# Optimization experiments

Hardware: AMD Instinct MI355X
Metric: run time of the kernel (lower is better)

The kernel has to match this reference:

```python
import jax, jax.numpy as jnp
import numpy as np

VNUM = 50000
D = 256
NE = 1600000


def setup_inputs() -> dict:
    key = jax.random.key(0)
    ks = jax.random.split(key, 10)
    return {
        "vrepr": jax.random.normal(ks[0], (VNUM, D), dtype=jnp.float32) * 0.1,
        "sidx": jax.random.randint(ks[1], (NE,), 0, VNUM, dtype=jnp.int32),
        "tidx": jax.random.randint(ks[2], (NE,), 0, VNUM, dtype=jnp.int32),
        "esgn": jnp.where(jax.random.uniform(ks[3], (NE,)) < 0.5, -1.0, 1.0).astype(jnp.float32),
        "enorm": jax.random.uniform(ks[4], (NE,), dtype=jnp.float32),
        "loc_w": jax.random.normal(ks[5], (D, D), dtype=jnp.float32) / np.sqrt(D),
        "loc_b": jax.random.normal(ks[6], (D,), dtype=jnp.float32) * 0.01,
        "std_w": jax.random.normal(ks[7], (D, D), dtype=jnp.float32) / np.sqrt(D),
        "std_b": jax.random.normal(ks[8], (D,), dtype=jnp.float32) * 0.01,
        "eps": jax.random.normal(ks[9], (VNUM, D), dtype=jnp.float32),
    }


def reference(vrepr, sidx, tidx, esgn, enorm, loc_w, loc_b, std_w, std_b, eps):
    # GraphConv: gather source node features, weight by enorm*esgn, scatter-add to targets
    w = (enorm * esgn)[:, None]              # [E, 1]
    msg = vrepr[sidx] * w                    # [E, D]
    ptr = jax.ops.segment_sum(msg, tidx, num_segments=vrepr.shape[0])  # [V, D]
    # Linear heads (torch Linear: y = x @ W.T + b)
    loc = ptr @ loc_w.T + loc_b
    std = jax.nn.softplus(ptr @ std_w.T + std_b) + 1e-7
    # rsample: loc + std * eps
    vsample = loc + std * eps
    return loc, std, vsample
```

## Files before the change

### kernel.cpp

```cpp
#include <hip/hip_runtime.h>

#define D 256

typedef __attribute__((ext_vector_type(8))) short s16x8;
typedef __attribute__((ext_vector_type(4))) float f32x4;

static __device__ __forceinline__ unsigned short f2b(float f) {
    unsigned u = __float_as_uint(f);
    unsigned r = (u + 0x7fffu + ((u >> 16) & 1u)) >> 16;
    return (unsigned short)r;
}
static __device__ __forceinline__ unsigned pack2(float a, float b) {
    return (unsigned)f2b(a) | ((unsigned)f2b(b) << 16);
}

static __device__ __forceinline__ void gload_lds16(const void* g, void* l) {
    __builtin_amdgcn_global_load_lds((const __attribute__((address_space(1))) unsigned int*)g,
                                     (__attribute__((address_space(3))) unsigned int*)l,
                                     16, 0, 0);
}

__global__ void prep_w_kernel(const float* __restrict__ lw, const float* __restrict__ sw,
                              unsigned short* __restrict__ wTf) {
    int i = blockIdx.x * 256 + threadIdx.x;
    float v = (i < D * D) ? lw[i] : sw[i - D * D];
    int n = i >> 8;
    int k = i & 255;
    int lane = (n & 15) | (((k >> 3) & 3) << 4);
    int unit = ((n >> 4) << 9) + ((k >> 5) << 6) + lane;
    wTf[unit * 8 + (k & 7)] = f2b(v);
}

__global__ void conv_v_kernel(const float* __restrict__ vr, unsigned short* __restrict__ vb, int n8) {
    int i = blockIdx.x * 256 + threadIdx.x;
    if (i < n8) {
        float4 f0 = ((const float4*)vr)[2 * i];
        float4 f1 = ((const float4*)vr)[2 * i + 1];
        uint4 o;
        o.x = pack2(f0.x, f0.y);
        o.y = pack2(f0.z, f0.w);
        o.z = pack2(f1.x, f1.y);
        o.w = pack2(f1.z, f1.w);
        ((uint4*)vb)[i] = o;
    }
}

__global__ void hist_kernel(const int* __restrict__ tidx, int* __restrict__ cnt,
                            int* __restrict__ rank, int E) {
    int e = blockIdx.x * blockDim.x + threadIdx.x;
    if (e < E) rank[e] = atomicAdd(&cnt[tidx[e]], 1);
}

__global__ void scan1_kernel(const int* __restrict__ cnt, int* __restrict__ bsum, int V) {
    __shared__ int red[256];
    int b = blockIdx.x, tid = threadIdx.x;
    int base = b * 1024 + tid * 4;
    int s = 0;
    if (base + 3 < V) {
        int4 q = *(const int4*)&cnt[base];
        s = q.x + q.y + q.z + q.w;
    } else {
        for (int j = 0; j < 4; ++j)
            if (base + j < V) s += cnt[base + j];
    }
    red[tid] = s;
    __syncthreads();
    for (int ofs = 128; ofs > 0; ofs >>= 1) {
        if (tid < ofs) red[tid] += red[tid + ofs];
        __syncthreads();
    }
    if (tid == 0) bsum[b] = red[0];
}

__global__ void scan2_kernel(int* __restrict__ bsum, int nb) {
    __shared__ int s[256];
    int tid = threadIdx.x;
    int v = (tid < nb) ? bsum[tid] : 0;
    s[tid] = v;
    __syncthreads();
    for (int ofs = 1; ofs < 256; ofs <<= 1) {
        int t = (tid >= ofs) ? s[tid - ofs] : 0;
        __syncthreads();
        s[tid] += t;
        __syncthreads();
    }
    if (tid < nb) bsum[tid] = s[tid] - v;
}

__global__ void scan3_kernel(const int* __restrict__ cnt, const int* __restrict__ bsum,
                             int* __restrict__ off, int V, int E) {
    __shared__ int ts[256];
    int b = blockIdx.x, tid = threadIdx.x;
    int base = b * 1024 + tid * 4;
    int v0 = 0, v1 = 0, v2 = 0, v3 = 0;
    if (base + 3 < V) {
        int4 q = *(const int4*)&cnt[base];
        v0 = q.x; v1 = q.y; v2 = q.z; v3 = q.w;
    } else {
        if (base < V)     v0 = cnt[base];
        if (base + 1 < V) v1 = cnt[base + 1];
        if (base + 2 < V) v2 = cnt[base + 2];
        if (base + 3 < V) v3 = cnt[base + 3];
    }
    int tsum = v0 + v1 + v2 + v3;
    ts[tid] = tsum;
    __syncthreads();
    for (int ofs = 1; ofs < 256; ofs <<= 1) {
        int t = (tid >= ofs) ? ts[tid - ofs] : 0;
        __syncthreads();
        ts[tid] += t;
        __syncthreads();
    }
    int pre = bsum[b] + ts[tid] - tsum;
    if (base + 3 < V) {
        int4 o = make_int4(pre, pre + v0, pre + v0 + v1, pre + v0 + v1 + v2);
        *(int4*)&off[base] = o;
    } else {
        if (base < V)     off[base] = pre;
        if (base + 1 < V) off[base + 1] = pre + v0;
        if (base + 2 < V) off[base + 2] = pre + v0 + v1;
        if (base + 3 < V) off[base + 3] = pre + v0 + v1 + v2;
    }
    if (b == 0 && tid == 0) off[V] = E;
}

__global__ void fill_kernel(const int* __restrict__ sidx, const int* __restrict__ tidx,
                            const float* __restrict__ esgn, const float* __restrict__ enorm,
                            const int* __restrict__ off, const int* __restrict__ rank,
                            int2* __restrict__ pk, int E) {
    int e = blockIdx.x * blockDim.x + threadIdx.x;
    if (e >= E) return;
    int idx = off[tidx[e]] + rank[e];
    float w = enorm[e] * esgn[e];
    pk[idx] = make_int2(sidx[e], __float_as_int(w));
}

#define FMA8(A, W)                                                   \
    acc[0] = fmaf(__uint_as_float((A).x << 16), (W), acc[0]);        \
    acc[1] = fmaf(__uint_as_float((A).x & 0xffff0000u), (W), acc[1]);\
    acc[2] = fmaf(__uint_as_float((A).y << 16), (W), acc[2]);        \
    acc[3] = fmaf(__uint_as_float((A).y & 0xffff0000u), (W), acc[3]);\
    acc[4] = fmaf(__uint_as_float((A).z << 16), (W), acc[4]);        \
    acc[5] = fmaf(__uint_as_float((A).z & 0xffff0000u), (W), acc[5]);\
    acc[6] = fmaf(__uint_as_float((A).w << 16), (W), acc[6]);        \
    acc[7] = fmaf(__uint_as_float((A).w & 0xffff0000u), (W), acc[7]);

__global__ __launch_bounds__(256) void accum_kernel(const unsigned short* __restrict__ vb,
                                                    const int2* __restrict__ pk,
                                                    const int* __restrict__ off,
                                                    unsigned short* __restrict__ ptrf, int V) {
    int gid = blockIdx.x * blockDim.x + threadIdx.x;
    int v = gid >> 6;
    if (v >= V) return;
    int lane = threadIdx.x & 63;
    int half = lane >> 5;
    int c = lane & 31;
    int beg = off[v], end = off[v + 1];
    int mid = beg + ((end - beg + 1) >> 1);
    int i = half ? mid : beg;
    int e = half ? end : mid;
    const uint4* base = (const uint4*)vb;
    float acc[8];
#pragma unroll
    for (int j = 0; j < 8; ++j) acc[j] = 0.f;
    for (; i + 3 < e; i += 4) {
        int2 p0 = pk[i];
        int2 p1 = pk[i + 1];
        int2 p2 = pk[i + 2];
        int2 p3 = pk[i + 3];
        uint4 a0 = base[(size_t)p0.x * 32 + c];
        uint4 a1 = base[(size_t)p1.x * 32 + c];
        uint4 a2 = base[(size_t)p2.x * 32 + c];
        uint4 a3 = base[(size_t)p3.x * 32 + c];
        float w0 = __int_as_float(p0.y);
        float w1 = __int_as_float(p1.y);
        float w2 = __int_as_float(p2.y);
        float w3 = __int_as_float(p3.y);
        FMA8(a0, w0)
        FMA8(a1, w1)
        FMA8(a2, w2)
        FMA8(a3, w3)
    }
    for (; i < e; ++i) {
        int2 p = pk[i];
        float w = __int_as_float(p.y);
        uint4 a = base[(size_t)p.x * 32 + c];
        FMA8(a, w)
    }
#pragma unroll
    for (int j = 0; j < 8; ++j) acc[j] += __shfl_xor(acc[j], 32, 64);
    if (half == 0) {
        uint4 o;
        o.x = pack2(acc[0], acc[1]);
        o.y = pack2(acc[2], acc[3]);
        o.z = pack2(acc[4], acc[5]);
        o.w = pack2(acc[6], acc[7]);
        int fl = (v & 15) | ((c & 3) << 4);
        int unit = ((v >> 4) << 9) + ((c >> 2) << 6) + fl;
        ((uint4*)ptrf)[unit] = o;
    }
}

__global__ __launch_bounds__(256, 4) void head_mfma_kernel(const unsigned short* __restrict__ ptrf,
                                                           const unsigned short* __restrict__ wTf,
                                                           const float* __restrict__ lb,
                                                           const float* __restrict__ sb,
                                                           const float* __restrict__ eps,
                                                           float* __restrict__ out, int V) {
    __shared__ s16x8 Blds[2][1024];
    int tid = threadIdx.x;
    int wave = tid >> 6, lane = tid & 63;
    int nhalf = blockIdx.x;
    int nb = nhalf << 3;
    int mt = blockIdx.y * 4 + wave;
    int lastmt = (V - 1) >> 4;
    int mtc = mt > lastmt ? lastmt : mt;
    int v0 = mt << 4;

    const s16x8* Af = (const s16x8*)ptrf + ((size_t)mtc << 9) + lane;
    s16x8 a[8];
#pragma unroll
    for (int kt = 0; kt < 8; ++kt) a[kt] = Af[kt << 6];

    const s16x8* Bf = (const s16x8*)wTf;

    f32x4 acc[16];
    f32x4 zero = {0.f, 0.f, 0.f, 0.f};
#pragma unroll
    for (int nt = 0; nt < 16; ++nt) acc[nt] = zero;

#define STAGE_B(KT, BUF)                                                      \
    {                                                                         \
        _Pragma("unroll")                                                     \
        for (int j = 0; j < 4; ++j) {                                         \
            int ln = j * 4 + wave;                                            \
            int nt = (ln < 8) ? (nb + ln) : (16 + nb + (ln - 8));             \
            gload_lds16((const void*)(Bf + (nt << 9) + ((KT) << 6) + lane),   \
                        (void*)&Blds[BUF][ln << 6]);                          \
        }                                                                     \
    }

    STAGE_B(0, 0);
    __syncthreads();

#pragma unroll
    for (int kt = 0; kt < 8; ++kt) {
        int buf = kt & 1;
        if (kt < 7) STAGE_B(kt + 1, buf ^ 1);
#pragma unroll
        for (int ln = 0; ln < 16; ++ln) {
            s16x8 b = Blds[buf][(ln << 6) + lane];
            acc[ln] = __builtin_amdgcn_mfma_f32_16x16x32_bf16(a[kt], b, acc[ln], 0, 0, 0);
        }
        if (kt < 7) __syncthreads();
    }
#undef STAGE_B

    if (v0 < V) {
        int quad = lane >> 4, m16 = lane & 15;
        size_t VD = (size_t)V * D;
        const float* epsb = eps + (size_t)v0 * D;
        float* outb = out + (size_t)v0 * D;
#pragma unroll
        for (int ln = 0; ln < 8; ++ln) {
            int col = (nhalf << 7) + (ln << 4) + m16;
            float lbv = lb[col];
            float sbv = sb[col];
#pragma unroll
            for (int r = 0; r < 4; ++r) {
                int row = (quad << 2) + r;
                int o = row * D + col;
                float lo = acc[ln][r] + lbv;
                float pre = acc[ln + 8][r] + sbv;
                float sp = fmaxf(pre, 0.f) + __logf(1.f + __expf(-fabsf(pre)));
                float st = sp + 1e-7f;
                float ep = __builtin_nontemporal_load(&epsb[o]);
                outb[o] = lo;
                outb[VD + o] = st;
                outb[2 * VD + o] = fmaf(st, ep, lo);
            }
        }
    }
}

extern "C" void kernel_launch(void* const* d_in, const int* in_sizes, int n_in,
                              void* d_out, int out_size, void* d_ws, size_t ws_size,
                              hipStream_t stream) {
    const float* vrepr = (const float*)d_in[0];
    const int*   sidx  = (const int*)d_in[1];
    const int*   tidx  = (const int*)d_in[2];
    const float* esgn  = (const float*)d_in[3];
    const float* enorm = (const float*)d_in[4];
    const float* loc_w = (const float*)d_in[5];
    const float* loc_b = (const float*)d_in[6];
    const float* std_w = (const float*)d_in[7];
    const float* std_b = (const float*)d_in[8];
    const float* eps   = (const float*)d_in[9];
    float* out = (float*)d_out;

    int E = in_sizes[1];
    int V = in_sizes[0] / D;

    char* ws = (char*)d_ws;
    size_t o = 0;
    unsigned short* vb   = (unsigned short*)(ws + o); o += (size_t)V * D * 2;
    unsigned short* ptrf = (unsigned short*)(ws + o); o += (size_t)V * D * 2;
    unsigned short* wTf  = (unsigned short*)(ws + o); o += (size_t)2 * D * D * 2;
    int* off  = (int*)(ws + o); o += ((size_t)V + 16) * sizeof(int);
    int* cnt  = (int*)(ws + o); o += ((size_t)V + 16) * sizeof(int);
    int* rank = (int*)(ws + o); o += (size_t)E * sizeof(int);
    int* bsum = (int*)(ws + o); o += 256 * sizeof(int);
    o = (o + 15) & ~(size_t)15;
    int2* pk = (int2*)(ws + o); o += (size_t)E * sizeof(int2);

    int nb = (V + 1023) >> 10;

    hipMemsetAsync(cnt, 0, (size_t)V * sizeof(int), stream);
    prep_w_kernel<<<(2 * D * D) / 256, 256, 0, stream>>>(loc_w, std_w, wTf);
    conv_v_kernel<<<(V * (D / 8) + 255) / 256, 256, 0, stream>>>(vrepr, vb, V * (D / 8));
    hist_kernel<<<(E + 255) / 256, 256, 0, stream>>>(tidx, cnt, rank, E);
    scan1_kernel<<<nb, 256, 0, stream>>>(cnt, bsum, V);
    scan2_kernel<<<1, 256, 0, stream>>>(bsum, nb);
    scan3_kernel<<<nb, 256, 0, stream>>>(cnt, bsum, off, V, E);
    fill_kernel<<<(E + 255) / 256, 256, 0, stream>>>(sidx, tidx, esgn, enorm, off, rank, pk, E);
    accum_kernel<<<(V * 64 + 255) / 256, 256, 0, stream>>>(vb, pk, off, ptrf, V);
    dim3 hgrid(2, (V + 63) / 64);
    head_mfma_kernel<<<hgrid, 256, 0, stream>>>(ptrf, wTf, loc_b, std_b, eps, out, V);
}
```

Baseline: 525.2 us.

## Merge prep kernels, nontemporal edge records, triple-buffer head B staging

Fuses the weight-transpose and vrepr bf16 conversion into one launch and vectorizes the weight path to four elements per thread. Edge records are stored and loaded as 64-bit nontemporal values so they do not pollute cache needed for the gathered node rows, and accum_kernel gets a higher occupancy hint. The head GEMM moves from double to triple-buffered LDS staging, using explicit vmcnt waits and raw barriers instead of __syncthreads. This trades more LDS per block and hand-tuned wait counts for better overlap of loads with MFMA work.

```diff
diff --git a/kernel.cpp b/kernel.cpp
--- a/kernel.cpp
+++ b/kernel.cpp
@@ -20,28 +20,37 @@
                                      16, 0, 0);
 }
 
-__global__ void prep_w_kernel(const float* __restrict__ lw, const float* __restrict__ sw,
-                              unsigned short* __restrict__ wTf) {
-    int i = blockIdx.x * 256 + threadIdx.x;
-    float v = (i < D * D) ? lw[i] : sw[i - D * D];
-    int n = i >> 8;
-    int k = i & 255;
-    int lane = (n & 15) | (((k >> 3) & 3) << 4);
-    int unit = ((n >> 4) << 9) + ((k >> 5) << 6) + lane;
-    wTf[unit * 8 + (k & 7)] = f2b(v);
-}
-
-__global__ void conv_v_kernel(const float* __restrict__ vr, unsigned short* __restrict__ vb, int n8) {
-    int i = blockIdx.x * 256 + threadIdx.x;
-    if (i < n8) {
-        float4 f0 = ((const float4*)vr)[2 * i];
-        float4 f1 = ((const float4*)vr)[2 * i + 1];
-        uint4 o;
-        o.x = pack2(f0.x, f0.y);
-        o.y = pack2(f0.z, f0.w);
-        o.z = pack2(f1.x, f1.y);
-        o.w = pack2(f1.z, f1.w);
-        ((uint4*)vb)[i] = o;
+__global__ void prep_conv_kernel(const float* __restrict__ vr,
+                                 const float* __restrict__ lw, const float* __restrict__ sw,
+                                 unsigned short* __restrict__ vb,
+                                 unsigned short* __restrict__ wTf, int n8, int nvb) {
+    if ((int)blockIdx.x < nvb) {
+        int i = blockIdx.x * 256 + threadIdx.x;
+        if (i < n8) {
+            float4 f0 = ((const float4*)vr)[2 * i];
+            float4 f1 = ((const float4*)vr)[2 * i + 1];
+            uint4 o;
+            o.x = pack2(f0.x, f0.y);
+            o.y = pack2(f0.z, f0.w);
+            o.z = pack2(f1.x, f1.y);
+            o.w = pack2(f1.z, f1.w);
+            ((uint4*)vb)[i] = o;
+        }
+    } else {
+        int i = (blockIdx.x - nvb) * 256 + threadIdx.x;
+        int e0 = i * 4;
+        if (e0 < 2 * D * D) {
+            const float* src = (e0 < D * D) ? (lw + e0) : (sw + (e0 - D * D));
+            float4 f = *(const float4*)src;
+            int n = e0 >> 8;
+            int k0 = e0 & 255;
+            int lane = (n & 15) | (((k0 >> 3) & 3) << 4);
+            int unit = ((n >> 4) << 9) + ((k0 >> 5) << 6) + lane;
+            uint2 o;
+            o.x = pack2(f.x, f.y);
+            o.y = pack2(f.z, f.w);
+            *(uint2*)&wTf[unit * 8 + (k0 & 7)] = o;
+        }
     }
 }
 
@@ -127,12 +136,14 @@
 __global__ void fill_kernel(const int* __restrict__ sidx, const int* __restrict__ tidx,
                             const float* __restrict__ esgn, const float* __restrict__ enorm,
                             const int* __restrict__ off, const int* __restrict__ rank,
-                            int2* __restrict__ pk, int E) {
+                            long long* __restrict__ pk, int E) {
     int e = blockIdx.x * blockDim.x + threadIdx.x;
     if (e >= E) return;
     int idx = off[tidx[e]] + rank[e];
     float w = enorm[e] * esgn[e];
-    pk[idx] = make_int2(sidx[e], __float_as_int(w));
+    long long rec = (long long)(unsigned)sidx[e] |
+                    ((long long)(unsigned)__float_as_uint(w) << 32);
+    __builtin_nontemporal_store(rec, &pk[idx]);
 }
 
 #define FMA8(A, W)                                                   \
@@ -145,10 +156,10 @@
     acc[6] = fmaf(__uint_as_float((A).w << 16), (W), acc[6]);        \
     acc[7] = fmaf(__uint_as_float((A).w & 0xffff0000u), (W), acc[7]);
 
-__global__ __launch_bounds__(256) void accum_kernel(const unsigned short* __restrict__ vb,
-                                                    const int2* __restrict__ pk,
-                                                    const int* __restrict__ off,
-                                                    unsigned short* __restrict__ ptrf, int V) {
+__global__ __launch_bounds__(256, 8) void accum_kernel(const unsigned short* __restrict__ vb,
+                                                       const long long* __restrict__ pk,
+                                                       const int* __restrict__ off,
+                                                       unsigned short* __restrict__ ptrf, int V) {
     int gid = blockIdx.x * blockDim.x + threadIdx.x;
     int v = gid >> 6;
     if (v >= V) return;
@@ -164,27 +175,27 @@
 #pragma unroll
     for (int j = 0; j < 8; ++j) acc[j] = 0.f;
     for (; i + 3 < e; i += 4) {
-        int2 p0 = pk[i];
-        int2 p1 = pk[i + 1];
-        int2 p2 = pk[i + 2];
-        int2 p3 = pk[i + 3];
-        uint4 a0 = base[(size_t)p0.x * 32 + c];
-        uint4 a1 = base[(size_t)p1.x * 32 + c];
-        uint4 a2 = base[(size_t)p2.x * 32 + c];
-        uint4 a3 = base[(size_t)p3.x * 32 + c];
-        float w0 = __int_as_float(p0.y);
-        float w1 = __int_as_float(p1.y);
-        float w2 = __int_as_float(p2.y);
-        float w3 = __int_as_float(p3.y);
+        long long r0 = __builtin_nontemporal_load(&pk[i]);
+        long long r1 = __builtin_nontemporal_load(&pk[i + 1]);
+        long long r2 = __builtin_nontemporal_load(&pk[i + 2]);
+        long long r3 = __builtin_nontemporal_load(&pk[i + 3]);
+        uint4 a0 = base[(size_t)(unsigned)r0 * 32 + c];
+        uint4 a1 = base[(size_t)(unsigned)r1 * 32 + c];
+        uint4 a2 = base[(size_t)(unsigned)r2 * 32 + c];
+        uint4 a3 = base[(size_t)(unsigned)r3 * 32 + c];
+        float w0 = __uint_as_float((unsigned)((unsigned long long)r0 >> 32));
+        float w1 = __uint_as_float((unsigned)((unsigned long long)r1 >> 32));
+        float w2 = __uint_as_float((unsigned)((unsigned long long)r2 >> 32));
+        float w3 = __uint_as_float((unsigned)((unsigned long long)r3 >> 32));
         FMA8(a0, w0)
         FMA8(a1, w1)
         FMA8(a2, w2)
         FMA8(a3, w3)
     }
     for (; i < e; ++i) {
-        int2 p = pk[i];
-        float w = __int_as_float(p.y);
-        uint4 a = base[(size_t)p.x * 32 + c];
+        long long r = __builtin_nontemporal_load(&pk[i]);
+        float w = __uint_as_float((unsigned)((unsigned long long)r >> 32));
+        uint4 a = base[(size_t)(unsigned)r * 32 + c];
         FMA8(a, w)
     }
 #pragma unroll
@@ -207,7 +218,7 @@
                                                            const float* __restrict__ sb,
                                                            const float* __restrict__ eps,
                                                            float* __restrict__ out, int V) {
-    __shared__ s16x8 Blds[2][1024];
+    __shared__ s16x8 Blds[3][1024];
     int tid = threadIdx.x;
     int wave = tid >> 6, lane = tid & 63;
     int nhalf = blockIdx.x;
@@ -241,18 +252,23 @@
     }
 
     STAGE_B(0, 0);
-    __syncthreads();
+    STAGE_B(1, 1);
 
 #pragma unroll
     for (int kt = 0; kt < 8; ++kt) {
-        int buf = kt & 1;
-        if (kt < 7) STAGE_B(kt + 1, buf ^ 1);
+        int buf = kt % 3;
+        if (kt < 6) STAGE_B(kt + 2, (kt + 2) % 3);
+        if (kt < 6)       asm volatile("s_waitcnt vmcnt(8)" ::: "memory");
+        else if (kt == 6) asm volatile("s_waitcnt vmcnt(4)" ::: "memory");
+        else              asm volatile("s_waitcnt vmcnt(0)" ::: "memory");
+        __builtin_amdgcn_sched_barrier(0);
+        __builtin_amdgcn_s_barrier();
 #pragma unroll
         for (int ln = 0; ln < 16; ++ln) {
             s16x8 b = Blds[buf][(ln << 6) + lane];
             acc[ln] = __builtin_amdgcn_mfma_f32_16x16x32_bf16(a[kt], b, acc[ln], 0, 0, 0);
         }
-        if (kt < 7) __syncthreads();
+        if (kt < 7) __builtin_amdgcn_s_barrier();
     }
 #undef STAGE_B
 
@@ -311,13 +327,15 @@
     int* rank = (int*)(ws + o); o += (size_t)E * sizeof(int);
     int* bsum = (int*)(ws + o); o += 256 * sizeof(int);
     o = (o + 15) & ~(size_t)15;
-    int2* pk = (int2*)(ws + o); o += (size_t)E * sizeof(int2);
+    long long* pk = (long long*)(ws + o); o += (size_t)E * sizeof(long long);
 
     int nb = (V + 1023) >> 10;
+    int n8 = V * (D / 8);
+    int nvb = (n8 + 255) / 256;
+    int nwb = (2 * D * D + 1023) / 1024;
 
     hipMemsetAsync(cnt, 0, (size_t)V * sizeof(int), stream);
-    prep_w_kernel<<<(2 * D * D) / 256, 256, 0, stream>>>(loc_w, std_w, wTf);
-    conv_v_kernel<<<(V * (D / 8) + 255) / 256, 256, 0, stream>>>(vrepr, vb, V * (D / 8));
+    prep_conv_kernel<<<nvb + nwb, 256, 0, stream>>>(vrepr, loc_w, std_w, vb, wTf, n8, nvb);
     hist_kernel<<<(E + 255) / 256, 256, 0, stream>>>(tidx, cnt, rank, E);
     scan1_kernel<<<nb, 256, 0, stream>>>(cnt, bsum, V);
     scan2_kernel<<<1, 256, 0, stream>>>(bsum, nb);
```

Result: slower. 582.0 us (+10.8%).
